# Optimization experiments

Hardware: AMD Instinct MI355X
Metric: run time of the kernel (lower is better)

The kernel has to match this reference:

```python
import jax, jax.numpy as jnp
import numpy as np

D_MODEL = 512
NHEAD = 8
HEAD_DIM = D_MODEL // NHEAD
WINDOW = 128


def setup_inputs() -> dict:
    key = jax.random.key(0)
    ks = jax.random.split(key, 5)
    B, S = 2, 2048
    scale = D_MODEL ** -0.5
    return {
        "x": jax.random.normal(ks[0], (B, S, D_MODEL), dtype=jnp.float32),
        # weights stored [in, out] so y = x @ W (equivalent to nn.Linear, bias=False)
        "Wq": jax.random.normal(ks[1], (D_MODEL, D_MODEL), dtype=jnp.float32) * scale,
        "Wk": jax.random.normal(ks[2], (D_MODEL, D_MODEL), dtype=jnp.float32) * scale,
        "Wv": jax.random.normal(ks[3], (D_MODEL, D_MODEL), dtype=jnp.float32) * scale,
        "Wo": jax.random.normal(ks[4], (D_MODEL, D_MODEL), dtype=jnp.float32) * scale,
    }


def reference(x, Wq, Wk, Wv, Wo):
    B, S, _ = x.shape
    # projections -> [B, H, S, D]
    def split_heads(y):
        return y.reshape(B, S, NHEAD, HEAD_DIM).transpose(0, 2, 1, 3)
    q = split_heads(x @ Wq)
    k = split_heads(x @ Wk)
    v = split_heads(x @ Wv)

    # causal sliding window: position p attends to [p - WINDOW + 1, p]
    pos = jnp.arange(S)
    offs = jnp.arange(WINDOW)
    idx = pos[:, None] - (WINDOW - 1) + offs[None, :]          # [S, W]
    valid = idx >= 0                                            # mask out-of-range (padded) slots
    idxc = jnp.clip(idx, 0, S - 1)

    k_w = k[:, :, idxc]                                         # [B, H, S, W, D]
    v_w = v[:, :, idxc]                                         # [B, H, S, W, D]

    inv_sqrt_d = jnp.float32(1.0 / np.sqrt(HEAD_DIM))
    scores = jnp.einsum('bhsd,bhswd->bhsw', q, k_w) * inv_sqrt_d
    scores = jnp.where(valid[None, None], scores, -jnp.inf)    # same as torch -inf masking of pads
    attn = jax.nn.softmax(scores, axis=-1)                      # last slot (self) always valid
    out = jnp.einsum('bhsw,bhswd->bhsd', attn, v_w)             # [B, H, S, D]
    out = out.transpose(0, 2, 1, 3).reshape(B, S, D_MODEL)
    return out @ Wo
```

## Files before the change

kernel.cpp:

```cpp
#include <hip/hip_runtime.h>

typedef __attribute__((ext_vector_type(8))) short bf16x8;
typedef __attribute__((ext_vector_type(4))) float f32x4;

#define D_MODEL 512
#define SEQ 2048
#define NHEAD 8
#define WIN 128

__device__ inline unsigned short f2bf(float f) {
    unsigned u = __float_as_uint(f);
    unsigned r = (u + 0x7fffu + ((u >> 16) & 1u)) >> 16;
    return (unsigned short)r;
}

__device__ inline void async_load16(const void* g, void* l) {
    __builtin_amdgcn_global_load_lds((const __attribute__((address_space(1))) void*)g,
                                     (__attribute__((address_space(3))) void*)l, 16, 0, 0);
}

__global__ __launch_bounds__(256) void prep(const float* __restrict__ x,
                                            const float* __restrict__ Wq,
                                            const float* __restrict__ Wk,
                                            const float* __restrict__ Wv,
                                            const float* __restrict__ Wo,
                                            unsigned short* __restrict__ xc,
                                            unsigned short* __restrict__ Wt) {
    __shared__ float tile[32 * 33];
    const int t = threadIdx.x;
    if (blockIdx.x < 2048) {
        int i = blockIdx.x * 256 + t;
        float4 v = ((const float4*)x)[i];
        ushort4 o;
        o.x = f2bf(v.x); o.y = f2bf(v.y); o.z = f2bf(v.z); o.w = f2bf(v.w);
        ((ushort4*)xc)[i] = o;
        return;
    }
    int idx = blockIdx.x - 2048;
    const int mat = idx >> 8;
    const int rem = idx & 255;
    const int ti = rem & 15, tj = rem >> 4;
    const float* W = mat == 0 ? Wq : mat == 1 ? Wk : mat == 2 ? Wv : Wo;
    {
        int c = t & 31, r4 = (t >> 5) * 4;
        #pragma unroll
        for (int e = 0; e < 4; e++)
            tile[(r4 + e) * 33 + c] = W[(size_t)(ti * 32 + r4 + e) * 512 + tj * 32 + c];
    }
    __syncthreads();
    {
        int rr = t & 31, c4 = (t >> 5) * 4;
        #pragma unroll
        for (int e = 0; e < 4; e++)
            Wt[(size_t)mat * 262144 + (size_t)(tj * 32 + c4 + e) * 512 + ti * 32 + rr] =
                f2bf(tile[rr * 33 + c4 + e]);
    }
}

__device__ inline void storeC(float* C, size_t i, float v) { C[i] = v; }
__device__ inline void storeC(unsigned short* C, size_t i, float v) { C[i] = f2bf(v); }

template <typename OUT, int NT>
__global__ __launch_bounds__(256) void gemm64(const unsigned short* __restrict__ A,
                                              const unsigned short* __restrict__ Bt,
                                              OUT* __restrict__ C, int Nstride) {
    __shared__ unsigned short As[64 * 32];
    __shared__ unsigned short Bs[NT * 16 * 32];
    const int t = threadIdx.x;
    const int w = t >> 6, l = t & 63;
    const int mBase = blockIdx.x * 64;
    const int nBase = blockIdx.y * (NT * 16);
    const int r0 = t >> 2, koff = (t & 3) * 8;
    const unsigned short* a0 = A + (size_t)(mBase + r0) * 512 + koff;
    const unsigned short* b0 = Bt + (size_t)(nBase + r0) * 512 + koff;
    const unsigned short* b1 = Bt + (size_t)(nBase + 64 + r0) * 512 + koff;
    unsigned short* asd  = &As[t * 8];
    unsigned short* bsd0 = &Bs[t * 8];
    unsigned short* bsd1 = &Bs[2048 + t * 8];

    const int lm = l & 15;
    const int kg = (l >> 4) * 8;

    f32x4 acc[NT];
    #pragma unroll
    for (int j = 0; j < NT; j++) acc[j] = (f32x4){0.f, 0.f, 0.f, 0.f};

    for (int k0 = 0; k0 < 512; k0 += 32) {
        async_load16(a0 + k0, asd);
        async_load16(b0 + k0, bsd0);
        if (NT == 8) async_load16(b1 + k0, bsd1);
        __syncthreads();
        bf16x8 af = *(const bf16x8*)&As[(w * 16 + lm) * 32 + kg];
        #pragma unroll
        for (int j = 0; j < NT; j++) {
            bf16x8 bfr = *(const bf16x8*)&Bs[(j * 16 + lm) * 32 + kg];
            acc[j] = __builtin_amdgcn_mfma_f32_16x16x32_bf16(af, bfr, acc[j], 0, 0, 0);
        }
        __syncthreads();
    }
    const int rRow = (l >> 4) * 4;
    const int cCol = l & 15;
    #pragma unroll
    for (int j = 0; j < NT; j++)
        #pragma unroll
        for (int r = 0; r < 4; r++) {
            size_t row = (size_t)(mBase + w * 16 + rRow + r);
            size_t col = (size_t)(nBase + j * 16 + cCol);
            storeC(C, row * (size_t)Nstride + col, acc[j][r]);
        }
}

__global__ __launch_bounds__(256) void attn_mfma(const unsigned short* __restrict__ QKV,
                                                 unsigned short* __restrict__ AO) {
    __shared__ unsigned short Ks[192 * 72];
    __shared__ unsigned short Qs[64 * 72];
    __shared__ unsigned short Vs[64 * 200];
    __shared__ unsigned short Pb[4][16 * 40];

    const int t = threadIdx.x;
    const int w = t >> 6, l = t & 63;
    const int s0 = blockIdx.x * 64;
    const int h = blockIdx.y, b = blockIdx.z;
    const unsigned short* base = QKV + (size_t)b * SEQ * 1536;

    for (int i = t; i < 192 * 8; i += 256) {
        int j = i >> 3, c8 = i & 7;
        int g = s0 - 127 + j;
        g = g < 0 ? 0 : (g > SEQ - 1 ? SEQ - 1 : g);
        *(uint4*)&Ks[j * 72 + c8 * 8] =
            *(const uint4*)(base + (size_t)g * 1536 + 512 + h * 64 + c8 * 8);
    }
    for (int i = t; i < 64 * 8; i += 256) {
        int r = i >> 3, c8 = i & 7;
        *(uint4*)&Qs[r * 72 + c8 * 8] =
            *(const uint4*)(base + (size_t)(s0 + r) * 1536 + h * 64 + c8 * 8);
    }
    for (int i = t; i < 192 * 8; i += 256) {
        int j = i >> 3, c8 = i & 7;
        int g = s0 - 127 + j;
        g = g < 0 ? 0 : (g > SEQ - 1 ? SEQ - 1 : g);
        uint4 vv = *(const uint4*)(base + (size_t)g * 1536 + 1024 + h * 64 + c8 * 8);
        unsigned short e16[8];
        *(uint4*)e16 = vv;
        int chunk = (j >> 3) ^ c8;
        int off = chunk * 8 + (j & 7);
        #pragma unroll
        for (int e = 0; e < 8; e++)
            Vs[(c8 * 8 + e) * 200 + off] = e16[e];
    }
    __syncthreads();

    const int lm = l & 15, lk = (l >> 4) * 8;

    f32x4 sc[12];
    #pragma unroll
    for (int kb = 0; kb < 12; kb++) sc[kb] = (f32x4){0.f, 0.f, 0.f, 0.f};
    bf16x8 aq[2];
    #pragma unroll
    for (int ks = 0; ks < 2; ks++)
        aq[ks] = *(const bf16x8*)&Qs[(w * 16 + lm) * 72 + ks * 32 + lk];
    #pragma unroll
    for (int kb = 0; kb < 12; kb++) {
        #pragma unroll
        for (int ks = 0; ks < 2; ks++) {
            bf16x8 bk = *(const bf16x8*)&Ks[(kb * 16 + lm) * 72 + ks * 32 + lk];
            sc[kb] = __builtin_amdgcn_mfma_f32_16x16x32_bf16(aq[ks], bk, sc[kb], 0, 0, 0);
        }
    }

    const int qr0 = (l >> 4) * 4;
    const int jlo_g = 127 - s0;
    float mrow[4] = {-1e30f, -1e30f, -1e30f, -1e30f};
    #pragma unroll
    for (int kb = 0; kb < 12; kb++) {
        int j = kb * 16 + lm;
        #pragma unroll
        for (int r = 0; r < 4; r++) {
            int qi = w * 16 + qr0 + r;
            bool valid = (j >= qi) & (j <= qi + 127) & (j >= jlo_g);
            float v = valid ? sc[kb][r] * 0.125f : -1e30f;
            sc[kb][r] = v;
            mrow[r] = fmaxf(mrow[r], v);
        }
    }
    #pragma unroll
    for (int r = 0; r < 4; r++) {
        mrow[r] = fmaxf(mrow[r], __shfl_xor(mrow[r], 1));
        mrow[r] = fmaxf(mrow[r], __shfl_xor(mrow[r], 2));
        mrow[r] = fmaxf(mrow[r], __shfl_xor(mrow[r], 4));
        mrow[r] = fmaxf(mrow[r], __shfl_xor(mrow[r], 8));
    }
    float srow[4] = {0.f, 0.f, 0.f, 0.f};
    #pragma unroll
    for (int kb = 0; kb < 12; kb++)
        #pragma unroll
        for (int r = 0; r < 4; r++) {
            float p = __expf(sc[kb][r] - mrow[r]);
            sc[kb][r] = p;
            srow[r] += p;
        }
    #pragma unroll
    for (int r = 0; r < 4; r++) {
        srow[r] += __shfl_xor(srow[r], 1);
        srow[r] += __shfl_xor(srow[r], 2);
        srow[r] += __shfl_xor(srow[r], 4);
        srow[r] += __shfl_xor(srow[r], 8);
        srow[r] = 1.f / srow[r];
    }

    f32x4 ov[4];
    #pragma unroll
    for (int nb = 0; nb < 4; nb++) ov[nb] = (f32x4){0.f, 0.f, 0.f, 0.f};
    unsigned short* pb = &Pb[w][0];
    #pragma unroll
    for (int c = 0; c < 6; c++) {
        #pragma unroll
        for (int kk = 0; kk < 2; kk++)
            #pragma unroll
            for (int r = 0; r < 4; r++)
                pb[(qr0 + r) * 40 + kk * 16 + lm] = f2bf(sc[2 * c + kk][r]);
        bf16x8 ap = *(const bf16x8*)&pb[lm * 40 + lk];
        #pragma unroll
        for (int nb = 0; nb < 4; nb++) {
            int d = nb * 16 + lm;
            int cj = c * 4 + (l >> 4);
            int off = ((cj ^ ((d >> 3) & 7)) * 8);
            bf16x8 bv = *(const bf16x8*)&Vs[d * 200 + off];
            ov[nb] = __builtin_amdgcn_mfma_f32_16x16x32_bf16(ap, bv, ov[nb], 0, 0, 0);
        }
    }

    #pragma unroll
    for (int nb = 0; nb < 4; nb++)
        #pragma unroll
        for (int r = 0; r < 4; r++) {
            size_t row = (size_t)(b * SEQ + s0 + w * 16 + qr0 + r);
            AO[row * 512 + h * 64 + nb * 16 + lm] = f2bf(ov[nb][r] * srow[r]);
        }
}

extern "C" void kernel_launch(void* const* d_in, const int* in_sizes, int n_in,
                              void* d_out, int out_size, void* d_ws, size_t ws_size,
                              hipStream_t stream) {
    const float* x  = (const float*)d_in[0];
    const float* Wq = (const float*)d_in[1];
    const float* Wk = (const float*)d_in[2];
    const float* Wv = (const float*)d_in[3];
    const float* Wo = (const float*)d_in[4];
    float* out = (float*)d_out;

    char* ws = (char*)d_ws;
    unsigned short* xc  = (unsigned short*)ws;
    unsigned short* Wt  = (unsigned short*)(ws + 4u * 1024 * 1024);
    unsigned short* QKV = (unsigned short*)(ws + 6u * 1024 * 1024);
    unsigned short* AO  = (unsigned short*)(ws + 18u * 1024 * 1024);

    prep<<<3072, 256, 0, stream>>>(x, Wq, Wk, Wv, Wo, xc, Wt);
    gemm64<unsigned short, 8><<<dim3(64, 12), 256, 0, stream>>>(xc, Wt, QKV, 1536);
    attn_mfma<<<dim3(32, 8, 2), 256, 0, stream>>>(QKV, AO);
    gemm64<float, 4><<<dim3(64, 8), 256, 0, stream>>>(AO, Wt + 3 * 262144, out, 512);
}
```

Measured before the change: 104.4 us.

## Double GEMM K-step to 64 with XOR-swizzled LDS and async attention loads

The GEMM now stages a 64-wide K slice per iteration, which halves the number of loop iterations and barriers. It loads into LDS with an XOR swizzle so the MFMA fragment reads avoid bank conflicts without padding. The attention kernel replaces its synchronous register-staged K and Q loads with direct global-to-LDS async loads, using the same swizzled unpadded layout. This trades more LDS per GEMM block, which could lower occupancy, for fewer syncs and cheaper loads.

```diff
diff --git a/kernel.cpp b/kernel.cpp
--- a/kernel.cpp
+++ b/kernel.cpp
@@ -64,76 +64,91 @@
 __global__ __launch_bounds__(256) void gemm64(const unsigned short* __restrict__ A,
                                               const unsigned short* __restrict__ Bt,
                                               OUT* __restrict__ C, int Nstride) {
-    __shared__ unsigned short As[64 * 32];
-    __shared__ unsigned short Bs[NT * 16 * 32];
+    __shared__ unsigned short As[64 * 64];
+    __shared__ unsigned short Bs[NT * 16 * 64];
     const int t = threadIdx.x;
     const int w = t >> 6, l = t & 63;
+    const int lm = l & 15;
     const int mBase = blockIdx.x * 64;
     const int nBase = blockIdx.y * (NT * 16);
-    const int r0 = t >> 2, koff = (t & 3) * 8;
-    const unsigned short* a0 = A + (size_t)(mBase + r0) * 512 + koff;
-    const unsigned short* b0 = Bt + (size_t)(nBase + r0) * 512 + koff;
-    const unsigned short* b1 = Bt + (size_t)(nBase + 64 + r0) * 512 + koff;
-    unsigned short* asd  = &As[t * 8];
-    unsigned short* bsd0 = &Bs[t * 8];
-    unsigned short* bsd1 = &Bs[2048 + t * 8];
-
-    const int lm = l & 15;
-    const int kg = (l >> 4) * 8;
+
+    const unsigned short* aptr[2];
+    #pragma unroll
+    for (int n = 0; n < 2; n++) {
+        int s = t + n * 256;
+        int r = s >> 3, lc = (s & 7) ^ (r & 7);
+        aptr[n] = A + (size_t)(mBase + r) * 512 + lc * 8;
+    }
+    const unsigned short* bptr[NT / 2];
+    #pragma unroll
+    for (int n = 0; n < NT / 2; n++) {
+        int s = t + n * 256;
+        int r = s >> 3, lc = (s & 7) ^ (r & 7);
+        bptr[n] = Bt + (size_t)(nBase + r) * 512 + lc * 8;
+    }
 
     f32x4 acc[NT];
     #pragma unroll
     for (int j = 0; j < NT; j++) acc[j] = (f32x4){0.f, 0.f, 0.f, 0.f};
 
-    for (int k0 = 0; k0 < 512; k0 += 32) {
-        async_load16(a0 + k0, asd);
-        async_load16(b0 + k0, bsd0);
-        if (NT == 8) async_load16(b1 + k0, bsd1);
+    for (int k0 = 0; k0 < 512; k0 += 64) {
+        #pragma unroll
+        for (int n = 0; n < 2; n++) async_load16(aptr[n] + k0, &As[(t + n * 256) * 8]);
+        #pragma unroll
+        for (int n = 0; n < NT / 2; n++) async_load16(bptr[n] + k0, &Bs[(t + n * 256) * 8]);
         __syncthreads();
-        bf16x8 af = *(const bf16x8*)&As[(w * 16 + lm) * 32 + kg];
-        #pragma unroll
-        for (int j = 0; j < NT; j++) {
-            bf16x8 bfr = *(const bf16x8*)&Bs[(j * 16 + lm) * 32 + kg];
-            acc[j] = __builtin_amdgcn_mfma_f32_16x16x32_bf16(af, bfr, acc[j], 0, 0, 0);
+        #pragma unroll
+        for (int ks = 0; ks < 2; ks++) {
+            const int koff = (((ks * 4 + (l >> 4)) ^ (lm & 7)) * 8);
+            bf16x8 af = *(const bf16x8*)&As[(w * 16 + lm) * 64 + koff];
+            #pragma unroll
+            for (int j = 0; j < NT; j++) {
+                bf16x8 bfr = *(const bf16x8*)&Bs[(j * 16 + lm) * 64 + koff];
+                acc[j] = __builtin_amdgcn_mfma_f32_16x16x32_bf16(af, bfr, acc[j], 0, 0, 0);
+            }
         }
         __syncthreads();
     }
     const int rRow = (l >> 4) * 4;
-    const int cCol = l & 15;
     #pragma unroll
     for (int j = 0; j < NT; j++)
         #pragma unroll
         for (int r = 0; r < 4; r++) {
             size_t row = (size_t)(mBase + w * 16 + rRow + r);
-            size_t col = (size_t)(nBase + j * 16 + cCol);
+            size_t col = (size_t)(nBase + j * 16 + lm);
             storeC(C, row * (size_t)Nstride + col, acc[j][r]);
         }
 }
 
 __global__ __launch_bounds__(256) void attn_mfma(const unsigned short* __restrict__ QKV,
                                                  unsigned short* __restrict__ AO) {
-    __shared__ unsigned short Ks[192 * 72];
-    __shared__ unsigned short Qs[64 * 72];
+    __shared__ unsigned short Ks[192 * 64];
+    __shared__ unsigned short Qs[64 * 64];
     __shared__ unsigned short Vs[64 * 200];
     __shared__ unsigned short Pb[4][16 * 40];
 
     const int t = threadIdx.x;
     const int w = t >> 6, l = t & 63;
+    const int lm = l & 15;
     const int s0 = blockIdx.x * 64;
     const int h = blockIdx.y, b = blockIdx.z;
     const unsigned short* base = QKV + (size_t)b * SEQ * 1536;
 
-    for (int i = t; i < 192 * 8; i += 256) {
+    #pragma unroll
+    for (int n = 0; n < 6; n++) {
+        int i = t + n * 256;
         int j = i >> 3, c8 = i & 7;
+        int lc = c8 ^ (j & 7);
         int g = s0 - 127 + j;
         g = g < 0 ? 0 : (g > SEQ - 1 ? SEQ - 1 : g);
-        *(uint4*)&Ks[j * 72 + c8 * 8] =
-            *(const uint4*)(base + (size_t)g * 1536 + 512 + h * 64 + c8 * 8);
-    }
-    for (int i = t; i < 64 * 8; i += 256) {
-        int r = i >> 3, c8 = i & 7;
-        *(uint4*)&Qs[r * 72 + c8 * 8] =
-            *(const uint4*)(base + (size_t)(s0 + r) * 1536 + h * 64 + c8 * 8);
+        async_load16(base + (size_t)g * 1536 + 512 + h * 64 + lc * 8, &Ks[i * 8]);
+    }
+    #pragma unroll
+    for (int n = 0; n < 2; n++) {
+        int i = t + n * 256;
+        int j = i >> 3, c8 = i & 7;
+        int lc = c8 ^ (j & 7);
+        async_load16(base + (size_t)(s0 + j) * 1536 + h * 64 + lc * 8, &Qs[i * 8]);
     }
     for (int i = t; i < 192 * 8; i += 256) {
         int j = i >> 3, c8 = i & 7;
@@ -150,21 +165,18 @@
     }
     __syncthreads();
 
-    const int lm = l & 15, lk = (l >> 4) * 8;
-
     f32x4 sc[12];
     #pragma unroll
     for (int kb = 0; kb < 12; kb++) sc[kb] = (f32x4){0.f, 0.f, 0.f, 0.f};
-    bf16x8 aq[2];
-    #pragma unroll
-    for (int ks = 0; ks < 2; ks++)
-        aq[ks] = *(const bf16x8*)&Qs[(w * 16 + lm) * 72 + ks * 32 + lk];
-    #pragma unroll
-    for (int kb = 0; kb < 12; kb++) {
-        #pragma unroll
-        for (int ks = 0; ks < 2; ks++) {
-            bf16x8 bk = *(const bf16x8*)&Ks[(kb * 16 + lm) * 72 + ks * 32 + lk];
-            sc[kb] = __builtin_amdgcn_mfma_f32_16x16x32_bf16(aq[ks], bk, sc[kb], 0, 0, 0);
+    #pragma unroll
+    for (int ks = 0; ks < 2; ks++) {
+        const int cq = ks * 4 + (l >> 4);
+        bf16x8 aq = *(const bf16x8*)&Qs[(w * 16 + lm) * 64 + ((cq ^ (lm & 7)) * 8)];
+        #pragma unroll
+        for (int kb = 0; kb < 12; kb++) {
+            int row = kb * 16 + lm;
+            bf16x8 bk = *(const bf16x8*)&Ks[row * 64 + ((cq ^ (row & 7)) * 8)];
+            sc[kb] = __builtin_amdgcn_mfma_f32_16x16x32_bf16(aq, bk, sc[kb], 0, 0, 0);
         }
     }
 
@@ -219,7 +231,7 @@
             #pragma unroll
             for (int r = 0; r < 4; r++)
                 pb[(qr0 + r) * 40 + kk * 16 + lm] = f2bf(sc[2 * c + kk][r]);
-        bf16x8 ap = *(const bf16x8*)&pb[lm * 40 + lk];
+        bf16x8 ap = *(const bf16x8*)&pb[lm * 40 + (l >> 4) * 8];
         #pragma unroll
         for (int nb = 0; nb < 4; nb++) {
             int d = nb * 16 + lm;
```

Result: faster. 99.99 us (median of 2 runs) (-4.2%).
